# Kernel tuning notes

Measured on AMD Instinct MI355X. Metric: run time of the kernel, lower is better.

## Reference

```python
import jax, jax.numpy as jnp
import numpy as np

B, S, H, DH = 2, 2048, 16, 64
D = H * DH


def setup_inputs() -> dict:
    key = jax.random.key(0)
    ks = jax.random.split(key, 10)
    std = 0.02
    return {
        "hidden_states": jax.random.normal(ks[0], (B, S, D), jnp.float32),
        "mask": jax.random.randint(ks[1], (B, S), 0, 2, jnp.int64 if jax.config.jax_enable_x64 else jnp.int32),
        "Wq": jax.random.normal(ks[2], (D, D), jnp.float32) * std,
        "bq": jnp.zeros((D,), jnp.float32),
        "Wk": jax.random.normal(ks[3], (D, D), jnp.float32) * std,
        "bk": jnp.zeros((D,), jnp.float32),
        "Wv": jax.random.normal(ks[4], (D, D), jnp.float32) * std,
        "bv": jnp.zeros((D,), jnp.float32),
        "Wo": jax.random.normal(ks[5], (D, D), jnp.float32) * std,
        "bo": jnp.zeros((D,), jnp.float32),
    }


def _split_heads(x):
    # (B, S, H*DH) -> (B, H, S, DH)
    b, s, _ = x.shape
    return x.reshape(b, s, H, DH).transpose(0, 2, 1, 3)


def reference(hidden_states, mask, Wq, bq, Wk, bk, Wv, bv, Wo, bo):
    # Linear projections (torch nn.Linear: x @ W.T + b)
    q = _split_heads(hidden_states @ Wq.T + bq)
    k = _split_heads(hidden_states @ Wk.T + bk)
    v = _split_heads(hidden_states @ Wv.T + bv)

    scale = 1.0 / np.sqrt(DH).astype(np.float32)
    scores = jnp.einsum("bhqd,bhkd->bhqk", q, k) * scale  # (B,H,S,S)
    # mask out padded key positions (mask==0 -> -inf), broadcast over heads/queries
    scores = jnp.where(mask[:, None, None, :] == 0, -jnp.inf, scores)
    weights = jax.nn.softmax(scores, axis=-1)

    attended = jnp.einsum("bhqk,bhkd->bhqd", weights, v)  # (B,H,S,DH)
    merged = attended.transpose(0, 2, 1, 3).reshape(hidden_states.shape)  # (B,S,D)
    return merged @ Wo.T + bo
```

## Files before the change

kernel.cpp:

```cpp
#include <hip/hip_runtime.h>
#include <hip/hip_bf16.h>

typedef __bf16 bf16;
typedef __bf16 bf16x4 __attribute__((ext_vector_type(4)));
typedef __bf16 bf16x8 __attribute__((ext_vector_type(8)));
typedef float f32x4 __attribute__((ext_vector_type(4)));

#define B_ 2
#define S_ 2048
#define H_ 16
#define DH_ 64
#define D_ 1024
#define NT_ 4096

#define WAIT_VMCNT0() asm volatile("s_waitcnt vmcnt(0)" ::: "memory")
#define WAIT_LGKM0()  asm volatile("s_waitcnt lgkmcnt(0)" ::: "memory")

__device__ __forceinline__ void gld_lds16(const bf16* g, bf16* l) {
    __builtin_amdgcn_global_load_lds(
        (__attribute__((address_space(1))) void*)g,
        (__attribute__((address_space(3))) void*)l, 16, 0, 0);
}

__device__ __forceinline__ bf16 f2bf(float x) {
    union { float f; unsigned u; } v; v.f = x;
    unsigned short h = (unsigned short)((v.u + 0x7FFF + ((v.u >> 16) & 1)) >> 16);
    return __builtin_bit_cast(bf16, h);
}

__global__ __launch_bounds__(256) void cvt_kernel(
    const float* __restrict__ hs,
    const float* __restrict__ Wq, const float* __restrict__ Wk,
    const float* __restrict__ Wv, const float* __restrict__ Wo,
    bf16* __restrict__ hsb, bf16* __restrict__ wqkv, bf16* __restrict__ wob)
{
    int i = (blockIdx.x * 256 + threadIdx.x) * 4;
    const float* src;
    bf16* dst;
    if (i < 4194304) {
        src = hs + i; dst = hsb + i;
    } else if (i < 7340032) {
        int off = i - 4194304;
        int which = off >> 20;
        int within = off & 1048575;
        src = (which == 0 ? Wq : which == 1 ? Wk : Wv) + within;
        dst = wqkv + off;
    } else {
        int off = i - 7340032;
        src = Wo + off; dst = wob + off;
    }
    float4 v = *(const float4*)src;
    bf16x4 o = { (bf16)v.x, (bf16)v.y, (bf16)v.z, (bf16)v.w };
    *(bf16x4*)dst = o;
}

__global__ __launch_bounds__(256, 2) void gemm_bt(
    const bf16* __restrict__ A, const bf16* __restrict__ Bm,
    int mode,
    const float* __restrict__ b0, const float* __restrict__ b1,
    const float* __restrict__ b2,
    bf16* __restrict__ Qo, bf16* __restrict__ Ko, bf16* __restrict__ Vt,
    float* __restrict__ Co)
{
    const int K = 1024;
    __shared__ __attribute__((aligned(16))) bf16 sA[128 * 32];
    __shared__ __attribute__((aligned(16))) bf16 sB[128 * 32];

    int tid = threadIdx.x;
    int wave = tid >> 6, lane = tid & 63;
    int quad = lane >> 4, l16 = lane & 15;
    int m0 = blockIdx.x * 128;
    int n0 = blockIdx.y * 128;
    int wm = (wave & 1) * 64, wn = (wave >> 1) * 64;
    int fs = (l16 >> 1) & 3;

    f32x4 acc[4][4];
#pragma unroll
    for (int i = 0; i < 4; i++)
#pragma unroll
        for (int j = 0; j < 4; j++) acc[i][j] = (f32x4){0.f, 0.f, 0.f, 0.f};

    for (int k0 = 0; k0 < K; k0 += 32) {
#pragma unroll
        for (int i = 0; i < 2; i++) {
            int chunk = tid + i * 256;
            int row = chunk >> 2;
            int kc = ((chunk & 3) ^ ((row >> 1) & 3)) * 8;
            gld_lds16(A + (size_t)(m0 + row) * K + k0 + kc, &sA[chunk * 8]);
            gld_lds16(Bm + (size_t)(n0 + row) * K + k0 + kc, &sB[chunk * 8]);
        }
        WAIT_VMCNT0();
        __syncthreads();

        bf16x8 af[4], bfr[4];
#pragma unroll
        for (int i = 0; i < 4; i++)
            af[i] = *(const bf16x8*)&sA[(wm + i * 16 + l16) * 32 + (quad ^ fs) * 8];
#pragma unroll
        for (int j = 0; j < 4; j++)
            bfr[j] = *(const bf16x8*)&sB[(wn + j * 16 + l16) * 32 + (quad ^ fs) * 8];
#pragma unroll
        for (int i = 0; i < 4; i++)
#pragma unroll
            for (int j = 0; j < 4; j++)
                acc[i][j] = __builtin_amdgcn_mfma_f32_16x16x32_bf16(
                    af[i], bfr[j], acc[i][j], 0, 0, 0);
        __syncthreads();
    }

    if (mode == 0) {
        const float QSCALE = 0.125f * 1.44269504088896340736f;
#pragma unroll
        for (int j = 0; j < 4; j++) {
            int n = n0 + wn + j * 16 + l16;
            int region = n >> 10;
            int nn = n & 1023;
            int h = nn >> 6, d = nn & 63;
            float bias = (region == 0 ? b0 : region == 1 ? b1 : b2)[nn];
#pragma unroll
            for (int i = 0; i < 4; i++)
#pragma unroll
                for (int r = 0; r < 4; r++) {
                    int m = m0 + wm + i * 16 + quad * 4 + r;
                    int b = m >> 11, s = m & 2047;
                    int bh = b * H_ + h;
                    float v = acc[i][j][r] + bias;
                    if (region == 0)
                        Qo[((size_t)bh * S_ + s) * DH_ + d] = f2bf(v * QSCALE);
                    else if (region == 1)
                        Ko[((size_t)bh * S_ + s) * DH_ + d] = f2bf(v);
                    else
                        Vt[((size_t)bh * DH_ + d) * S_ + s] = f2bf(v);
                }
        }
    } else {
#pragma unroll
        for (int j = 0; j < 4; j++) {
            int n = n0 + wn + j * 16 + l16;
            float bias = b0[n];
#pragma unroll
            for (int i = 0; i < 4; i++)
#pragma unroll
                for (int r = 0; r < 4; r++) {
                    int m = m0 + wm + i * 16 + quad * 4 + r;
                    Co[(size_t)m * D_ + n] = acc[i][j][r] + bias;
                }
        }
    }
}

__global__ __launch_bounds__(256, 2) void attn_kernel(
    const bf16* __restrict__ Q, const bf16* __restrict__ Kg,
    const bf16* __restrict__ Vt, const int* __restrict__ mask,
    bf16* __restrict__ Og)
{
    __shared__ __attribute__((aligned(16))) bf16 sK[64 * 64];
    __shared__ __attribute__((aligned(16))) bf16 sV[64 * 64];
    __shared__ __attribute__((aligned(16))) bf16 sP[4][32 * 64];
    __shared__ float sMaddAll[S_];

    int tid = threadIdx.x;
    int wave = tid >> 6, lane = tid & 63;
    int quad = lane >> 4, l16 = lane & 15;
    int bh = blockIdx.y;
    int b = bh >> 4;
    int q0 = blockIdx.x * 128;
    int f8 = l16 & 7;

    const bf16* Qb = Q + (size_t)bh * S_ * DH_;
    const bf16* Kb = Kg + (size_t)bh * S_ * DH_;
    const bf16* Vb = Vt + (size_t)bh * DH_ * S_;

#pragma unroll
    for (int i = 0; i < S_ / 256; i++) {
        int idx = tid + i * 256;
        sMaddAll[idx] = mask[b * S_ + idx] ? 0.f : -1e30f;
    }

    int chunk0 = tid, chunk1 = tid + 256;
    int krow0 = chunk0 >> 3, krow1 = chunk1 >> 3;
    int cc0 = ((chunk0 & 7) ^ (krow0 & 7)) * 8;
    int cc1 = ((chunk1 & 7) ^ (krow1 & 7)) * 8;

    bf16x8 aq[2][2];
#pragma unroll
    for (int m = 0; m < 2; m++) {
        int qrow = q0 + wave * 32 + m * 16 + l16;
        aq[m][0] = *(const bf16x8*)&Qb[(size_t)qrow * DH_ + quad * 8];
        aq[m][1] = *(const bf16x8*)&Qb[(size_t)qrow * DH_ + 32 + quad * 8];
    }

    f32x4 o[2][4];
#pragma unroll
    for (int m = 0; m < 2; m++)
#pragma unroll
        for (int i = 0; i < 4; i++) o[m][i] = (f32x4){0.f, 0.f, 0.f, 0.f};
    float psum[2][4] = {{0.f, 0.f, 0.f, 0.f}, {0.f, 0.f, 0.f, 0.f}};

    for (int kt = 0; kt < S_; kt += 64) {
        gld_lds16(&Kb[(size_t)(kt + krow0) * DH_ + cc0], &sK[chunk0 * 8]);
        gld_lds16(&Vb[(size_t)krow0 * S_ + kt + cc0], &sV[chunk0 * 8]);
        gld_lds16(&Kb[(size_t)(kt + krow1) * DH_ + cc1], &sK[chunk1 * 8]);
        gld_lds16(&Vb[(size_t)krow1 * S_ + kt + cc1], &sV[chunk1 * 8]);
        WAIT_VMCNT0();
        __syncthreads();

#pragma unroll
        for (int nt = 0; nt < 4; nt++) {
            bf16x8 bk0 = *(const bf16x8*)&sK[(nt * 16 + l16) * 64 + (quad ^ f8) * 8];
            bf16x8 bk1 = *(const bf16x8*)&sK[(nt * 16 + l16) * 64 + ((quad + 4) ^ f8) * 8];
            float ma = sMaddAll[kt + nt * 16 + l16];
#pragma unroll
            for (int m = 0; m < 2; m++) {
                f32x4 c = (f32x4){0.f, 0.f, 0.f, 0.f};
                c = __builtin_amdgcn_mfma_f32_16x16x32_bf16(aq[m][0], bk0, c, 0, 0, 0);
                c = __builtin_amdgcn_mfma_f32_16x16x32_bf16(aq[m][1], bk1, c, 0, 0, 0);
#pragma unroll
                for (int r = 0; r < 4; r++) {
                    float p = __builtin_amdgcn_exp2f(c[r] + ma);
                    psum[m][r] += p;
                    int row = quad * 4 + r;
                    int g = (nt * 2 + (l16 >> 3)) ^ (row & 7);
                    sP[wave][(m * 16 + row) * 64 + g * 8 + (l16 & 7)] = f2bf(p);
                }
            }
        }

        WAIT_LGKM0();
        bf16x8 ap[2][2];
#pragma unroll
        for (int m = 0; m < 2; m++) {
            ap[m][0] = *(const bf16x8*)&sP[wave][(m * 16 + l16) * 64 + (quad ^ f8) * 8];
            ap[m][1] = *(const bf16x8*)&sP[wave][(m * 16 + l16) * 64 + ((quad + 4) ^ f8) * 8];
        }
#pragma unroll
        for (int dt = 0; dt < 4; dt++) {
            bf16x8 bv0 = *(const bf16x8*)&sV[(dt * 16 + l16) * 64 + (quad ^ f8) * 8];
            bf16x8 bv1 = *(const bf16x8*)&sV[(dt * 16 + l16) * 64 + ((quad + 4) ^ f8) * 8];
#pragma unroll
            for (int m = 0; m < 2; m++) {
                o[m][dt] = __builtin_amdgcn_mfma_f32_16x16x32_bf16(ap[m][0], bv0, o[m][dt], 0, 0, 0);
                o[m][dt] = __builtin_amdgcn_mfma_f32_16x16x32_bf16(ap[m][1], bv1, o[m][dt], 0, 0, 0);
            }
        }
        __syncthreads();
    }

    int h = bh & 15;
#pragma unroll
    for (int m = 0; m < 2; m++)
#pragma unroll
    for (int r = 0; r < 4; r++) {
        float v = psum[m][r];
        v += __shfl_xor(v, 1);
        v += __shfl_xor(v, 2);
        v += __shfl_xor(v, 4);
        v += __shfl_xor(v, 8);
        float rcp = 1.f / v;
        int s = q0 + wave * 32 + m * 16 + quad * 4 + r;
#pragma unroll
        for (int dt = 0; dt < 4; dt++) {
            int d = dt * 16 + l16;
            Og[((size_t)(b * S_ + s)) * D_ + h * 64 + d] = f2bf(o[m][dt][r] * rcp);
        }
    }
}

extern "C" void kernel_launch(void* const* d_in, const int* in_sizes, int n_in,
                              void* d_out, int out_size, void* d_ws, size_t ws_size,
                              hipStream_t stream) {
    const float* hs = (const float*)d_in[0];
    const int* mask = (const int*)d_in[1];
    const float* Wq = (const float*)d_in[2];
    const float* bq = (const float*)d_in[3];
    const float* Wk = (const float*)d_in[4];
    const float* bk = (const float*)d_in[5];
    const float* Wv = (const float*)d_in[6];
    const float* bv = (const float*)d_in[7];
    const float* Wo = (const float*)d_in[8];
    const float* bo = (const float*)d_in[9];
    float* out = (float*)d_out;

    char* ws = (char*)d_ws;
    bf16* hsb  = (bf16*)(ws);
    bf16* wqkv = (bf16*)(ws + ((size_t)8 << 20));
    bf16* wob  = (bf16*)(ws + ((size_t)14 << 20));
    bf16* Qw   = (bf16*)(ws + ((size_t)16 << 20));
    bf16* Kw   = (bf16*)(ws + ((size_t)24 << 20));
    bf16* Vtw  = (bf16*)(ws + ((size_t)32 << 20));
    bf16* attn = (bf16*)(ws + ((size_t)40 << 20));

    cvt_kernel<<<8192, 256, 0, stream>>>(hs, Wq, Wk, Wv, Wo, hsb, wqkv, wob);
    gemm_bt<<<dim3(32, 24), 256, 0, stream>>>(hsb, wqkv, 0, bq, bk, bv,
                                              Qw, Kw, Vtw, nullptr);
    attn_kernel<<<dim3(16, 32), 256, 0, stream>>>(Qw, Kw, Vtw, mask, attn);
    gemm_bt<<<dim3(32, 8), 256, 0, stream>>>(attn, wob, 1, bo, nullptr, nullptr,
                                             nullptr, nullptr, nullptr, out);
}
```

Baseline: 211.7 us.

## Restructure attention kernel into 128-key tiles with split-K waves and reduction

The attention kernel now loads 128-key K/V tiles per iteration. Its four waves are arranged as two query halves by two key halves, each wave covering 64 queries and 64 keys. Scores are computed transposed (K as the A operand), so each lane packs four probabilities into a bf16x4 store, and the row sums need only two cross-quad shuffles. At the end, partial outputs and sums from the key-half waves are reduced through shared memory. The aim is fewer barriers per key, more MFMA work per LDS load and cheaper softmax bookkeeping, at the cost of more LDS, more registers (16 accumulator tiles) and a final cross-wave reduction.

```diff
diff --git a/kernel.cpp b/kernel.cpp
--- a/kernel.cpp
+++ b/kernel.cpp
@@ -154,10 +154,12 @@
     const bf16* __restrict__ Vt, const int* __restrict__ mask,
     bf16* __restrict__ Og)
 {
-    __shared__ __attribute__((aligned(16))) bf16 sK[64 * 64];
-    __shared__ __attribute__((aligned(16))) bf16 sV[64 * 64];
-    __shared__ __attribute__((aligned(16))) bf16 sP[4][32 * 64];
+    __shared__ __attribute__((aligned(16))) bf16 sK[128 * 64];
+    __shared__ __attribute__((aligned(16))) bf16 sV[64 * 128];
+    __shared__ __attribute__((aligned(16))) bf16 sP[4][64 * 32];
     __shared__ float sMaddAll[S_];
+    __shared__ float sPsumR[128];
+    __shared__ float sPsumF[128];
 
     int tid = threadIdx.x;
     int wave = tid >> 6, lane = tid & 63;
@@ -166,6 +168,9 @@
     int b = bh >> 4;
     int q0 = blockIdx.x * 128;
     int f8 = l16 & 7;
+    int qh = wave & 1;
+    int kh = wave >> 1;
+    int X = (l16 & 6) ^ ((l16 & 8) >> 2);
 
     const bf16* Qb = Q + (size_t)bh * S_ * DH_;
     const bf16* Kb = Kg + (size_t)bh * S_ * DH_;
@@ -177,91 +182,128 @@
         sMaddAll[idx] = mask[b * S_ + idx] ? 0.f : -1e30f;
     }
 
-    int chunk0 = tid, chunk1 = tid + 256;
-    int krow0 = chunk0 >> 3, krow1 = chunk1 >> 3;
-    int cc0 = ((chunk0 & 7) ^ (krow0 & 7)) * 8;
-    int cc1 = ((chunk1 & 7) ^ (krow1 & 7)) * 8;
-
-    bf16x8 aq[2][2];
-#pragma unroll
-    for (int m = 0; m < 2; m++) {
-        int qrow = q0 + wave * 32 + m * 16 + l16;
-        aq[m][0] = *(const bf16x8*)&Qb[(size_t)qrow * DH_ + quad * 8];
-        aq[m][1] = *(const bf16x8*)&Qb[(size_t)qrow * DH_ + 32 + quad * 8];
-    }
-
-    f32x4 o[2][4];
-#pragma unroll
-    for (int m = 0; m < 2; m++)
-#pragma unroll
-        for (int i = 0; i < 4; i++) o[m][i] = (f32x4){0.f, 0.f, 0.f, 0.f};
-    float psum[2][4] = {{0.f, 0.f, 0.f, 0.f}, {0.f, 0.f, 0.f, 0.f}};
-
-    for (int kt = 0; kt < S_; kt += 64) {
-        gld_lds16(&Kb[(size_t)(kt + krow0) * DH_ + cc0], &sK[chunk0 * 8]);
-        gld_lds16(&Vb[(size_t)krow0 * S_ + kt + cc0], &sV[chunk0 * 8]);
-        gld_lds16(&Kb[(size_t)(kt + krow1) * DH_ + cc1], &sK[chunk1 * 8]);
-        gld_lds16(&Vb[(size_t)krow1 * S_ + kt + cc1], &sV[chunk1 * 8]);
+    bf16x8 aq[4][2];
+#pragma unroll
+    for (int qt = 0; qt < 4; qt++) {
+        int qrow = q0 + qh * 64 + qt * 16 + l16;
+        aq[qt][0] = *(const bf16x8*)&Qb[(size_t)qrow * DH_ + quad * 8];
+        aq[qt][1] = *(const bf16x8*)&Qb[(size_t)qrow * DH_ + 32 + quad * 8];
+    }
+
+    f32x4 o[4][4];
+#pragma unroll
+    for (int i = 0; i < 4; i++)
+#pragma unroll
+        for (int j = 0; j < 4; j++) o[i][j] = (f32x4){0.f, 0.f, 0.f, 0.f};
+    float psum[4] = {0.f, 0.f, 0.f, 0.f};
+
+    for (int kt = 0; kt < S_; kt += 128) {
+#pragma unroll
+        for (int i = 0; i < 8; i++) {
+            int c = tid + i * 256;
+            if (c < 1024) {
+                int row = c >> 3;
+                int g = (c & 7) ^ (row & 7);
+                gld_lds16(&Kb[(size_t)(kt + row) * DH_ + g * 8], &sK[c * 8]);
+            } else {
+                int cv = c - 1024;
+                int row = cv >> 4;
+                int g = (cv & 15) ^ (row & 15);
+                gld_lds16(&Vb[(size_t)row * S_ + kt + g * 8], &sV[cv * 8]);
+            }
+        }
         WAIT_VMCNT0();
         __syncthreads();
 
 #pragma unroll
-        for (int nt = 0; nt < 4; nt++) {
-            bf16x8 bk0 = *(const bf16x8*)&sK[(nt * 16 + l16) * 64 + (quad ^ f8) * 8];
-            bf16x8 bk1 = *(const bf16x8*)&sK[(nt * 16 + l16) * 64 + ((quad + 4) ^ f8) * 8];
-            float ma = sMaddAll[kt + nt * 16 + l16];
-#pragma unroll
-            for (int m = 0; m < 2; m++) {
-                f32x4 c = (f32x4){0.f, 0.f, 0.f, 0.f};
-                c = __builtin_amdgcn_mfma_f32_16x16x32_bf16(aq[m][0], bk0, c, 0, 0, 0);
-                c = __builtin_amdgcn_mfma_f32_16x16x32_bf16(aq[m][1], bk1, c, 0, 0, 0);
-#pragma unroll
-                for (int r = 0; r < 4; r++) {
-                    float p = __builtin_amdgcn_exp2f(c[r] + ma);
-                    psum[m][r] += p;
-                    int row = quad * 4 + r;
-                    int g = (nt * 2 + (l16 >> 3)) ^ (row & 7);
-                    sP[wave][(m * 16 + row) * 64 + g * 8 + (l16 & 7)] = f2bf(p);
+        for (int pass = 0; pass < 2; pass++) {
+#pragma unroll
+            for (int mtl = 0; mtl < 2; mtl++) {
+                int keyrow = kh * 64 + pass * 32 + mtl * 16;
+                bf16x8 ak0 = *(const bf16x8*)&sK[(keyrow + l16) * 64 + (quad ^ f8) * 8];
+                bf16x8 ak1 = *(const bf16x8*)&sK[(keyrow + l16) * 64 + ((quad + 4) ^ f8) * 8];
+                float4 ma4 = *(const float4*)&sMaddAll[kt + keyrow + quad * 4];
+#pragma unroll
+                for (int qt = 0; qt < 4; qt++) {
+                    f32x4 c = (f32x4){0.f, 0.f, 0.f, 0.f};
+                    c = __builtin_amdgcn_mfma_f32_16x16x32_bf16(ak0, aq[qt][0], c, 0, 0, 0);
+                    c = __builtin_amdgcn_mfma_f32_16x16x32_bf16(ak1, aq[qt][1], c, 0, 0, 0);
+                    float p0 = __builtin_amdgcn_exp2f(c[0] + ma4.x);
+                    float p1 = __builtin_amdgcn_exp2f(c[1] + ma4.y);
+                    float p2 = __builtin_amdgcn_exp2f(c[2] + ma4.z);
+                    float p3 = __builtin_amdgcn_exp2f(c[3] + ma4.w);
+                    psum[qt] += (p0 + p1) + (p2 + p3);
+                    bf16x4 pk = { f2bf(p0), f2bf(p1), f2bf(p2), f2bf(p3) };
+                    int g = (mtl * 4 + quad) ^ X;
+                    *(bf16x4*)&sP[wave][(qt * 16 + l16) * 32 + g * 4] = pk;
                 }
             }
-        }
-
+
+            WAIT_LGKM0();
+            bf16x8 ap[4];
+#pragma unroll
+            for (int qt = 0; qt < 4; qt++)
+                ap[qt] = *(const bf16x8*)&sP[wave][(qt * 16 + l16) * 32 + ((quad * 2) ^ X) * 4];
+#pragma unroll
+            for (int dt = 0; dt < 4; dt++) {
+                int g = (kh * 8 + pass * 4 + quad) ^ l16;
+                bf16x8 bv = *(const bf16x8*)&sV[(dt * 16 + l16) * 128 + g * 8];
+#pragma unroll
+                for (int qt = 0; qt < 4; qt++)
+                    o[qt][dt] = __builtin_amdgcn_mfma_f32_16x16x32_bf16(ap[qt], bv, o[qt][dt], 0, 0, 0);
+            }
+        }
+        __syncthreads();
+    }
+
+#pragma unroll
+    for (int qt = 0; qt < 4; qt++) {
+        float v = psum[qt];
+        v += __shfl_xor(v, 16);
+        v += __shfl_xor(v, 32);
+        psum[qt] = v;
+    }
+
+    __syncthreads();
+    float* sRed = (wave == 2) ? (float*)sK : (float*)sV;
+    if (wave >= 2) {
+#pragma unroll
+        for (int qt = 0; qt < 4; qt++)
+#pragma unroll
+            for (int dt = 0; dt < 4; dt++)
+                *(f32x4*)&sRed[((qt * 4 + dt) * 64 + lane) * 4] = o[qt][dt];
+#pragma unroll
+        for (int qt = 0; qt < 4; qt++)
+            sPsumR[(wave - 2) * 64 + qt * 16 + l16] = psum[qt];
+    }
+    __syncthreads();
+    if (wave < 2) {
+        float* src = (wave == 0) ? (float*)sK : (float*)sV;
+#pragma unroll
+        for (int qt = 0; qt < 4; qt++)
+#pragma unroll
+            for (int dt = 0; dt < 4; dt++)
+                o[qt][dt] += *(const f32x4*)&src[((qt * 4 + dt) * 64 + lane) * 4];
+#pragma unroll
+        for (int qt = 0; qt < 4; qt++) {
+            float v = psum[qt] + sPsumR[wave * 64 + qt * 16 + l16];
+            sPsumF[wave * 64 + qt * 16 + l16] = v;
+        }
         WAIT_LGKM0();
-        bf16x8 ap[2][2];
-#pragma unroll
-        for (int m = 0; m < 2; m++) {
-            ap[m][0] = *(const bf16x8*)&sP[wave][(m * 16 + l16) * 64 + (quad ^ f8) * 8];
-            ap[m][1] = *(const bf16x8*)&sP[wave][(m * 16 + l16) * 64 + ((quad + 4) ^ f8) * 8];
-        }
-#pragma unroll
-        for (int dt = 0; dt < 4; dt++) {
-            bf16x8 bv0 = *(const bf16x8*)&sV[(dt * 16 + l16) * 64 + (quad ^ f8) * 8];
-            bf16x8 bv1 = *(const bf16x8*)&sV[(dt * 16 + l16) * 64 + ((quad + 4) ^ f8) * 8];
-#pragma unroll
-            for (int m = 0; m < 2; m++) {
-                o[m][dt] = __builtin_amdgcn_mfma_f32_16x16x32_bf16(ap[m][0], bv0, o[m][dt], 0, 0, 0);
-                o[m][dt] = __builtin_amdgcn_mfma_f32_16x16x32_bf16(ap[m][1], bv1, o[m][dt], 0, 0, 0);
+        int h = bh & 15;
+#pragma unroll
+        for (int qt = 0; qt < 4; qt++) {
+            float4 ps = *(const float4*)&sPsumF[wave * 64 + qt * 16 + quad * 4];
+            float rcp[4] = { 1.f / ps.x, 1.f / ps.y, 1.f / ps.z, 1.f / ps.w };
+#pragma unroll
+            for (int r = 0; r < 4; r++) {
+                int s = q0 + qh * 64 + qt * 16 + quad * 4 + r;
+#pragma unroll
+                for (int dt = 0; dt < 4; dt++) {
+                    int d = dt * 16 + l16;
+                    Og[((size_t)(b * S_ + s)) * D_ + h * 64 + d] = f2bf(o[qt][dt][r] * rcp[r]);
+                }
             }
-        }
-        __syncthreads();
-    }
-
-    int h = bh & 15;
-#pragma unroll
-    for (int m = 0; m < 2; m++)
-#pragma unroll
-    for (int r = 0; r < 4; r++) {
-        float v = psum[m][r];
-        v += __shfl_xor(v, 1);
-        v += __shfl_xor(v, 2);
-        v += __shfl_xor(v, 4);
-        v += __shfl_xor(v, 8);
-        float rcp = 1.f / v;
-        int s = q0 + wave * 32 + m * 16 + quad * 4 + r;
-#pragma unroll
-        for (int dt = 0; dt < 4; dt++) {
-            int d = dt * 16 + l16;
-            Og[((size_t)(b * S_ + s)) * D_ + h * 64 + d] = f2bf(o[m][dt][r] * rcp);
         }
     }
 }
```

Result: faster. 205.9 us (-2.7%).
